# Kernel tuning notes

Measured on AMD Instinct MI355X. Metric: run time of the kernel, lower is better.

## Reference

```python
import jax, jax.numpy as jnp
import numpy as np

N = 100_000      # n_nodes
E = 1_000_000    # n_edges (avg degree 10)
DIN = 64
DOUT = 64


def setup_inputs() -> dict:
    key = jax.random.key(0)
    k1, k2, k3, k4 = jax.random.split(key, 4)
    x = jax.random.normal(k1, (N, DIN), dtype=jnp.float32)
    edge_index = jax.random.randint(k2, (2, E), 0, N, dtype=jnp.int32)
    # GCNConv linear weight (glorot-ish scale) and bias
    W = jax.random.normal(k3, (DIN, DOUT), dtype=jnp.float32) * (1.0 / np.sqrt(DIN))
    b = jax.random.normal(k4, (DOUT,), dtype=jnp.float32) * 0.01
    return {"x": x, "edge_index": edge_index, "W": W, "b": b}


def reference(x, edge_index, W, b):
    n = x.shape[0]
    # linear transform first (PyG GCNConv: x = self.lin(x))
    h = x @ W  # [N, DOUT]
    # add self-loops
    loop = jnp.arange(n, dtype=edge_index.dtype)
    row = jnp.concatenate([edge_index[0], loop])  # source j
    col = jnp.concatenate([edge_index[1], loop])  # target i
    # symmetric normalization: deg computed on target index (PyG gcn_norm)
    deg = jax.ops.segment_sum(jnp.ones(row.shape[0], dtype=h.dtype), col, num_segments=n)
    dinv = jnp.where(deg > 0, jax.lax.rsqrt(deg), 0.0)
    norm = dinv[row] * dinv[col]  # [E+N]
    # gather source features, scale, scatter-add to targets
    out = jax.ops.segment_sum(norm[:, None] * h[row], col, num_segments=n)
    out = out + b
    # dropout is identity in eval mode; act = relu
    return jax.nn.relu(out)
```

## Files before the change

### kernel.cpp

```cpp
#include <hip/hip_runtime.h>
#include <hip/hip_bf16.h>

#define F 64
#define BK 64
#define CAP 1024
#define ECAP 1024
#define KMAX 1600
#define PA_BLOCKS 512

typedef __attribute__((ext_vector_type(8))) short bf16x8;
typedef __attribute__((ext_vector_type(4))) float f32x4;

static __device__ inline short f2bf_bits(float f) {
    union { __hip_bfloat16 b; short s; } cv;
    cv.b = __float2bfloat16(f);
    return cv.s;
}

static __device__ inline float bf_lo(unsigned u) { return __uint_as_float(u << 16); }
static __device__ inline float bf_hi(unsigned u) { return __uint_as_float(u & 0xffff0000u); }

struct Acc8 {
    float a0, a1, a2, a3, a4, a5, a6, a7;
    __device__ inline void fma8(float wt, uint4 hv) {
        a0 += wt * bf_lo(hv.x);
        a1 += wt * bf_hi(hv.x);
        a2 += wt * bf_lo(hv.y);
        a3 += wt * bf_hi(hv.y);
        a4 += wt * bf_lo(hv.z);
        a5 += wt * bf_hi(hv.z);
        a6 += wt * bf_lo(hv.w);
        a7 += wt * bf_hi(hv.w);
    }
};

__global__ void __launch_bounds__(256)
k1_kernel(const float* __restrict__ x, const float* __restrict__ W,
          __hip_bfloat16* __restrict__ h,
          const int* __restrict__ row, const int* __restrict__ col,
          int* __restrict__ bcursor, unsigned* __restrict__ bin,
          int n, int e, int ngemm, int K, int chunk) {
    __shared__ int smem[2 * KMAX];
    int tid = threadIdx.x;

    if ((int)blockIdx.x < ngemm) {
        short* Wb = (short*)smem;
        for (int i = tid; i < F * F; i += 256) Wb[i] = f2bf_bits(W[i]);
        __syncthreads();
        int lane = tid & 63;
        int wv = tid >> 6;
        int quad = lane >> 4;
        int l16 = lane & 15;

        bf16x8 bfr[2][4];
#pragma unroll
        for (int ks = 0; ks < 2; ++ks)
#pragma unroll
            for (int nb = 0; nb < 4; ++nb) {
                bf16x8 f;
#pragma unroll
                for (int j = 0; j < 8; ++j)
                    f[j] = Wb[(ks * 32 + quad * 8 + j) * F + nb * 16 + l16];
                bfr[ks][nb] = f;
            }

        int blockbase = blockIdx.x * 128;
#pragma unroll
        for (int mt = 0; mt < 2; ++mt) {
            int trow = blockbase + (wv * 2 + mt) * 16;
            int ar = trow + l16;
            bf16x8 af0, af1;
            if (ar < n) {
                const float* xr = x + (size_t)ar * F + quad * 8;
                float4 v0 = ((const float4*)xr)[0];
                float4 v1 = ((const float4*)xr)[1];
                float4 v2 = ((const float4*)(xr + 32))[0];
                float4 v3 = ((const float4*)(xr + 32))[1];
                af0[0] = f2bf_bits(v0.x); af0[1] = f2bf_bits(v0.y);
                af0[2] = f2bf_bits(v0.z); af0[3] = f2bf_bits(v0.w);
                af0[4] = f2bf_bits(v1.x); af0[5] = f2bf_bits(v1.y);
                af0[6] = f2bf_bits(v1.z); af0[7] = f2bf_bits(v1.w);
                af1[0] = f2bf_bits(v2.x); af1[1] = f2bf_bits(v2.y);
                af1[2] = f2bf_bits(v2.z); af1[3] = f2bf_bits(v2.w);
                af1[4] = f2bf_bits(v3.x); af1[5] = f2bf_bits(v3.y);
                af1[6] = f2bf_bits(v3.z); af1[7] = f2bf_bits(v3.w);
            } else {
                af0 = (bf16x8)0; af1 = (bf16x8)0;
            }
            f32x4 acc[4];
#pragma unroll
            for (int nb = 0; nb < 4; ++nb) {
                acc[nb] = (f32x4)0.f;
                acc[nb] = __builtin_amdgcn_mfma_f32_16x16x32_bf16(af0, bfr[0][nb], acc[nb], 0, 0, 0);
                acc[nb] = __builtin_amdgcn_mfma_f32_16x16x32_bf16(af1, bfr[1][nb], acc[nb], 0, 0, 0);
            }
#pragma unroll
            for (int nb = 0; nb < 4; ++nb)
#pragma unroll
                for (int r = 0; r < 4; ++r) {
                    int grow = trow + quad * 4 + r;
                    if (grow < n)
                        h[(size_t)grow * F + nb * 16 + l16] = __float2bfloat16(acc[nb][r]);
                }
        }
    } else {
        int* lh = smem;
        int* lbase = smem + KMAX;
        int pb = blockIdx.x - ngemm;
        int s = pb * chunk;
        int lim = min(s + chunk, e);
        for (int i = tid; i < K; i += 256) lh[i] = 0;
        __syncthreads();
        for (int i = s + tid; i < lim; i += 256) atomicAdd(&lh[col[i] >> 6], 1);
        __syncthreads();
        for (int i = tid; i < K; i += 256) {
            int c = lh[i];
            lbase[i] = c ? atomicAdd(&bcursor[i], c) : 0;
            lh[i] = 0;
        }
        __syncthreads();
        for (int i = s + tid; i < lim; i += 256) {
            int d = col[i];
            int bkt = d >> 6;
            int off = lbase[bkt] + atomicAdd(&lh[bkt], 1);
            if (off < CAP)
                bin[(size_t)bkt * CAP + off] = ((unsigned)row[i] << 6) | ((unsigned)d & 63u);
        }
    }
}

__global__ void __launch_bounds__(256)
dinv_kernel(const unsigned* __restrict__ bin, const int* __restrict__ bcursor,
            float* __restrict__ dinv, int n) {
    __shared__ int lcnt[BK];
    int tid = threadIdx.x;
    int b = blockIdx.x;
    int s = b * CAP;
    int cnt = min(bcursor[b], ECAP);
    if (tid < BK) lcnt[tid] = 0;
    __syncthreads();
    for (int p = tid; p < cnt; p += 256) atomicAdd(&lcnt[bin[s + p] & 63u], 1);
    __syncthreads();
    if (tid < BK) {
        int node = (b << 6) + tid;
        if (node < n) dinv[node] = rsqrtf((float)(lcnt[tid] + 1));
    }
}

__global__ void __launch_bounds__(256)
gather_kernel(const unsigned* __restrict__ bin, const int* __restrict__ bcursor,
              const float* __restrict__ dinv, const __hip_bfloat16* __restrict__ h,
              const float* __restrict__ bias, float* __restrict__ out, int n) {
    __shared__ unsigned ebuf[ECAP];
    __shared__ uint2 sent[ECAP];
    __shared__ int lcnt[BK];
    __shared__ int sstart[BK];
    __shared__ int lcur[BK];
    __shared__ int sc[BK];
    __shared__ float sdinv[BK];
    int tid = threadIdx.x;
    int b = blockIdx.x;
    int base = b << 6;
    int s = b * CAP;
    int cnt = min(bcursor[b], ECAP);

    if (tid < BK) lcnt[tid] = 0;
    __syncthreads();
    for (int p = tid; p < cnt; p += 256) {
        unsigned u = bin[s + p];
        ebuf[p] = u;
        atomicAdd(&lcnt[u & 63u], 1);
    }
    __syncthreads();
    if (tid < BK) sc[tid] = lcnt[tid];
    __syncthreads();
    for (int off = 1; off < BK; off <<= 1) {
        int t = (tid < BK && tid >= off) ? sc[tid - off] : 0;
        __syncthreads();
        if (tid < BK) sc[tid] += t;
        __syncthreads();
    }
    if (tid < BK) {
        int c = lcnt[tid];
        int st = sc[tid] - c;
        sstart[tid] = st;
        lcur[tid] = st;
        sdinv[tid] = rsqrtf((float)(c + 1));
    }
    __syncthreads();
    for (int p = tid; p < cnt; p += 256) {
        unsigned u = ebuf[p];
        int src = (int)(u >> 6);
        float w = dinv[src];
        int pos = atomicAdd(&lcur[u & 63u], 1);
        sent[pos] = make_uint2((unsigned)src, __float_as_uint(w));
    }
    __syncthreads();

    int g = tid >> 3, cl = tid & 7;
    const uint4* h8 = (const uint4*)h;
#pragma unroll
    for (int r = 0; r < 2; ++r) {
        int ln = r * 32 + g;
        int node = base + ln;
        if (node >= n) continue;
        float di = sdinv[ln];
        Acc8 ac = {0.f, 0.f, 0.f, 0.f, 0.f, 0.f, 0.f, 0.f};
        {
            uint4 hv = h8[(size_t)node * 8 + cl];
            ac.fma8(di, hv);
        }
        int p = sstart[ln];
        int pend = p + lcnt[ln];
        for (; p + 4 <= pend; p += 4) {
            uint2 e0 = sent[p];
            uint2 e1 = sent[p + 1];
            uint2 e2 = sent[p + 2];
            uint2 e3 = sent[p + 3];
            uint4 v0 = h8[(size_t)e0.x * 8 + cl];
            uint4 v1 = h8[(size_t)e1.x * 8 + cl];
            uint4 v2 = h8[(size_t)e2.x * 8 + cl];
            uint4 v3 = h8[(size_t)e3.x * 8 + cl];
            ac.fma8(__uint_as_float(e0.y), v0);
            ac.fma8(__uint_as_float(e1.y), v1);
            ac.fma8(__uint_as_float(e2.y), v2);
            ac.fma8(__uint_as_float(e3.y), v3);
        }
        for (; p < pend; ++p) {
            uint2 ew = sent[p];
            uint4 hv = h8[(size_t)ew.x * 8 + cl];
            ac.fma8(__uint_as_float(ew.y), hv);
        }
        float4 b0 = ((const float4*)bias)[cl * 2];
        float4 b1 = ((const float4*)bias)[cl * 2 + 1];
        float4 r0, r1;
        r0.x = di * ac.a0 + b0.x; r0.y = di * ac.a1 + b0.y;
        r0.z = di * ac.a2 + b0.z; r0.w = di * ac.a3 + b0.w;
        r1.x = di * ac.a4 + b1.x; r1.y = di * ac.a5 + b1.y;
        r1.z = di * ac.a6 + b1.z; r1.w = di * ac.a7 + b1.w;
        r0.x = r0.x > 0.f ? r0.x : 0.f; r0.y = r0.y > 0.f ? r0.y : 0.f;
        r0.z = r0.z > 0.f ? r0.z : 0.f; r0.w = r0.w > 0.f ? r0.w : 0.f;
        r1.x = r1.x > 0.f ? r1.x : 0.f; r1.y = r1.y > 0.f ? r1.y : 0.f;
        r1.z = r1.z > 0.f ? r1.z : 0.f; r1.w = r1.w > 0.f ? r1.w : 0.f;
        ((float4*)out)[(size_t)node * 16 + cl * 2] = r0;
        ((float4*)out)[(size_t)node * 16 + cl * 2 + 1] = r1;
    }
}

extern "C" void kernel_launch(void* const* d_in, const int* in_sizes, int n_in,
                              void* d_out, int out_size, void* d_ws, size_t ws_size,
                              hipStream_t stream) {
    const float* x = (const float*)d_in[0];
    const int* ei  = (const int*)d_in[1];
    const float* W = (const float*)d_in[2];
    const float* b = (const float*)d_in[3];
    float* out = (float*)d_out;

    int n = in_sizes[0] / F;
    int e = in_sizes[1] / 2;
    const int* row = ei;
    const int* col = ei + e;
    int K = (n + BK - 1) / BK;

    __hip_bfloat16* h = (__hip_bfloat16*)d_ws;
    unsigned* bin = (unsigned*)((char*)d_ws + (size_t)n * F * 2);
    float* dinv   = (float*)(bin + (size_t)KMAX * CAP);
    int* bcursor  = (int*)(dinv + n);

    (void)hipMemsetAsync(bcursor, 0, KMAX * sizeof(int), stream);

    int ngemm = (n + 127) / 128;
    int chunk = (e + PA_BLOCKS - 1) / PA_BLOCKS;
    k1_kernel<<<ngemm + PA_BLOCKS, 256, 0, stream>>>(x, W, h, row, col, bcursor,
                                                     bin, n, e, ngemm, K, chunk);

    dinv_kernel<<<K, 256, 0, stream>>>(bin, bcursor, dinv, n);

    gather_kernel<<<K, 256, 0, stream>>>(bin, bcursor, dinv, h, b, out, n);
}
```

Before: 135.4 us.

## Privatize per-wave degree histograms, use shuffle scan, degree-sort nodes in gather

The degree histograms in dinv_kernel and gather_kernel are split into four per-wave copies to cut LDS atomic contention, then summed. The barrier-heavy shared-memory prefix scan is replaced by a wave-level __shfl_up scan. Each node is also ranked by degree and the gather loop walks nodes in that sorted order, so the 8-lane groups within a wave handle neighbor lists of similar length and diverge less. The cost is an extra O(64) rank loop per block and a little more shared memory.

```diff
diff --git a/kernel.cpp b/kernel.cpp
--- a/kernel.cpp
+++ b/kernel.cpp
@@ -132,18 +132,20 @@
 __global__ void __launch_bounds__(256)
 dinv_kernel(const unsigned* __restrict__ bin, const int* __restrict__ bcursor,
             float* __restrict__ dinv, int n) {
-    __shared__ int lcnt[BK];
+    __shared__ int lcnt4[4][BK];
     int tid = threadIdx.x;
     int b = blockIdx.x;
     int s = b * CAP;
     int cnt = min(bcursor[b], ECAP);
-    if (tid < BK) lcnt[tid] = 0;
-    __syncthreads();
-    for (int p = tid; p < cnt; p += 256) atomicAdd(&lcnt[bin[s + p] & 63u], 1);
+    ((int*)lcnt4)[tid] = 0;
+    __syncthreads();
+    int wvid = tid >> 6;
+    for (int p = tid; p < cnt; p += 256) atomicAdd(&lcnt4[wvid][bin[s + p] & 63u], 1);
     __syncthreads();
     if (tid < BK) {
+        int c = lcnt4[0][tid] + lcnt4[1][tid] + lcnt4[2][tid] + lcnt4[3][tid];
         int node = (b << 6) + tid;
-        if (node < n) dinv[node] = rsqrtf((float)(lcnt[tid] + 1));
+        if (node < n) dinv[node] = rsqrtf((float)(c + 1));
     }
 }
 
@@ -153,39 +155,46 @@
               const float* __restrict__ bias, float* __restrict__ out, int n) {
     __shared__ unsigned ebuf[ECAP];
     __shared__ uint2 sent[ECAP];
+    __shared__ int lcnt4[4][BK];
     __shared__ int lcnt[BK];
     __shared__ int sstart[BK];
     __shared__ int lcur[BK];
-    __shared__ int sc[BK];
     __shared__ float sdinv[BK];
+    __shared__ unsigned char order_[BK];
     int tid = threadIdx.x;
     int b = blockIdx.x;
     int base = b << 6;
     int s = b * CAP;
     int cnt = min(bcursor[b], ECAP);
-
-    if (tid < BK) lcnt[tid] = 0;
+    int wvid = tid >> 6;
+
+    ((int*)lcnt4)[tid] = 0;
     __syncthreads();
     for (int p = tid; p < cnt; p += 256) {
         unsigned u = bin[s + p];
         ebuf[p] = u;
-        atomicAdd(&lcnt[u & 63u], 1);
-    }
-    __syncthreads();
-    if (tid < BK) sc[tid] = lcnt[tid];
-    __syncthreads();
-    for (int off = 1; off < BK; off <<= 1) {
-        int t = (tid < BK && tid >= off) ? sc[tid - off] : 0;
-        __syncthreads();
-        if (tid < BK) sc[tid] += t;
-        __syncthreads();
-    }
+        atomicAdd(&lcnt4[wvid][u & 63u], 1);
+    }
+    __syncthreads();
     if (tid < BK) {
-        int c = lcnt[tid];
-        int st = sc[tid] - c;
+        int c = lcnt4[0][tid] + lcnt4[1][tid] + lcnt4[2][tid] + lcnt4[3][tid];
+        lcnt[tid] = c;
+        int scv = c;
+#pragma unroll
+        for (int off = 1; off < BK; off <<= 1) {
+            int t = __shfl_up(scv, off, 64);
+            if (tid >= off) scv += t;
+        }
+        int st = scv - c;
         sstart[tid] = st;
         lcur[tid] = st;
         sdinv[tid] = rsqrtf((float)(c + 1));
+        int rk = 0;
+        for (int j = 0; j < BK; ++j) {
+            int cj = lcnt[j];
+            rk += (cj < c) || (cj == c && j < tid);
+        }
+        order_[rk] = (unsigned char)tid;
     }
     __syncthreads();
     for (int p = tid; p < cnt; p += 256) {
@@ -201,7 +210,7 @@
     const uint4* h8 = (const uint4*)h;
 #pragma unroll
     for (int r = 0; r < 2; ++r) {
-        int ln = r * 32 + g;
+        int ln = order_[r * 32 + g];
         int node = base + ln;
         if (node >= n) continue;
         float di = sdinv[ln];
```

Result: slower. 141.8 us (+4.7%).

## Fold degree counting into first kernel with global atomics, drop dinv kernel

Applied to the files above, without the earlier changes.

Removes the separate dinv kernel launch by adding extra blocks to the fused GEMM/binning kernel that count in-degrees with global atomicAdd on col. The gather kernel then computes the source normalization as rsqrt(deg+1) on the fly instead of reading a precomputed dinv array. This saves one launch and one pass over the binned edges, but adds about a million global atomics that contend with the GEMM and binning blocks, plus a larger memset.

```diff
diff --git a/kernel.cpp b/kernel.cpp
--- a/kernel.cpp
+++ b/kernel.cpp
@@ -7,6 +7,7 @@
 #define ECAP 1024
 #define KMAX 1600
 #define PA_BLOCKS 512
+#define DEG_BLOCKS 256
 
 typedef __attribute__((ext_vector_type(8))) short bf16x8;
 typedef __attribute__((ext_vector_type(4))) float f32x4;
@@ -38,8 +39,9 @@
 k1_kernel(const float* __restrict__ x, const float* __restrict__ W,
           __hip_bfloat16* __restrict__ h,
           const int* __restrict__ row, const int* __restrict__ col,
-          int* __restrict__ bcursor, unsigned* __restrict__ bin,
-          int n, int e, int ngemm, int K, int chunk) {
+          int* __restrict__ bcursor, int* __restrict__ deg,
+          unsigned* __restrict__ bin,
+          int n, int e, int ngemm, int K, int chunk, int dchunk) {
     __shared__ int smem[2 * KMAX];
     int tid = threadIdx.x;
 
@@ -103,7 +105,7 @@
                         h[(size_t)grow * F + nb * 16 + l16] = __float2bfloat16(acc[nb][r]);
                 }
         }
-    } else {
+    } else if ((int)blockIdx.x < ngemm + PA_BLOCKS) {
         int* lh = smem;
         int* lbase = smem + KMAX;
         int pb = blockIdx.x - ngemm;
@@ -126,30 +128,18 @@
             if (off < CAP)
                 bin[(size_t)bkt * CAP + off] = ((unsigned)row[i] << 6) | ((unsigned)d & 63u);
         }
-    }
-}
-
-__global__ void __launch_bounds__(256)
-dinv_kernel(const unsigned* __restrict__ bin, const int* __restrict__ bcursor,
-            float* __restrict__ dinv, int n) {
-    __shared__ int lcnt[BK];
-    int tid = threadIdx.x;
-    int b = blockIdx.x;
-    int s = b * CAP;
-    int cnt = min(bcursor[b], ECAP);
-    if (tid < BK) lcnt[tid] = 0;
-    __syncthreads();
-    for (int p = tid; p < cnt; p += 256) atomicAdd(&lcnt[bin[s + p] & 63u], 1);
-    __syncthreads();
-    if (tid < BK) {
-        int node = (b << 6) + tid;
-        if (node < n) dinv[node] = rsqrtf((float)(lcnt[tid] + 1));
+    } else {
+        int db = blockIdx.x - ngemm - PA_BLOCKS;
+        int s = db * dchunk;
+        int lim = min(s + dchunk, e);
+        for (int i = s + tid; i < lim; i += 256)
+            atomicAdd(&deg[col[i]], 1);
     }
 }
 
 __global__ void __launch_bounds__(256)
 gather_kernel(const unsigned* __restrict__ bin, const int* __restrict__ bcursor,
-              const float* __restrict__ dinv, const __hip_bfloat16* __restrict__ h,
+              const int* __restrict__ deg, const __hip_bfloat16* __restrict__ h,
               const float* __restrict__ bias, float* __restrict__ out, int n) {
     __shared__ unsigned ebuf[ECAP];
     __shared__ uint2 sent[ECAP];
@@ -191,7 +181,7 @@
     for (int p = tid; p < cnt; p += 256) {
         unsigned u = ebuf[p];
         int src = (int)(u >> 6);
-        float w = dinv[src];
+        float w = rsqrtf((float)(deg[src] + 1));
         int pos = atomicAdd(&lcur[u & 63u], 1);
         sent[pos] = make_uint2((unsigned)src, __float_as_uint(w));
     }
@@ -264,17 +254,16 @@
 
     __hip_bfloat16* h = (__hip_bfloat16*)d_ws;
     unsigned* bin = (unsigned*)((char*)d_ws + (size_t)n * F * 2);
-    float* dinv   = (float*)(bin + (size_t)KMAX * CAP);
-    int* bcursor  = (int*)(dinv + n);
-
-    (void)hipMemsetAsync(bcursor, 0, KMAX * sizeof(int), stream);
+    int* deg      = (int*)(bin + (size_t)KMAX * CAP);
+    int* bcursor  = deg + n;
+
+    (void)hipMemsetAsync(deg, 0, (size_t)(n + KMAX) * sizeof(int), stream);
 
     int ngemm = (n + 127) / 128;
     int chunk = (e + PA_BLOCKS - 1) / PA_BLOCKS;
-    k1_kernel<<<ngemm + PA_BLOCKS, 256, 0, stream>>>(x, W, h, row, col, bcursor,
-                                                     bin, n, e, ngemm, K, chunk);
-
-    dinv_kernel<<<K, 256, 0, stream>>>(bin, bcursor, dinv, n);
-
-    gather_kernel<<<K, 256, 0, stream>>>(bin, bcursor, dinv, h, b, out, n);
-}
+    int dchunk = (e + DEG_BLOCKS - 1) / DEG_BLOCKS;
+    k1_kernel<<<ngemm + PA_BLOCKS + DEG_BLOCKS, 256, 0, stream>>>(
+        x, W, h, row, col, bcursor, deg, bin, n, e, ngemm, K, chunk, dchunk);
+
+    gather_kernel<<<K, 256, 0, stream>>>(bin, bcursor, deg, h, b, out, n);
+}
```

Result: slower. 170.3 us (+25.8%).

## Fuse dinv and gather kernels into one cooperative kernel with grid sync

Applied to the files above, without the earlier changes.

Replaces the separate dinv and gather launches with a single cooperative kernel. Each block reads its bucket's edges once into LDS, computes the degree and dinv, publishes dinv, waits on a grid-wide barrier, then gathers neighbour features. The aim is to cut one launch and the second global read of the bin array. In exchange it adds a grid sync and an occupancy query on the host, and the occupancy check (max blocks per CU times 256 against K) looks like an approximation that may not guarantee co-residency.

```diff
diff --git a/kernel.cpp b/kernel.cpp
--- a/kernel.cpp
+++ b/kernel.cpp
@@ -1,5 +1,8 @@
 #include <hip/hip_runtime.h>
 #include <hip/hip_bf16.h>
+#include <hip/hip_cooperative_groups.h>
+
+namespace cg = cooperative_groups;
 
 #define F 64
 #define BK 64
@@ -129,6 +132,105 @@
     }
 }
 
+__global__ void __launch_bounds__(256, 8)
+fused_kernel(const unsigned* __restrict__ bin, const int* __restrict__ bcursor,
+             float* __restrict__ dinv, const __hip_bfloat16* __restrict__ h,
+             const float* __restrict__ bias, float* __restrict__ out, int n) {
+    __shared__ unsigned ebuf[ECAP];
+    __shared__ uint2 sent[ECAP];
+    __shared__ int lcnt[BK];
+    __shared__ int sstart[BK];
+    __shared__ int lcur[BK];
+    __shared__ int sc[BK];
+    __shared__ float sdinv[BK];
+    int tid = threadIdx.x;
+    int b = blockIdx.x;
+    int base = b << 6;
+    int s = b * CAP;
+    int cnt = min(bcursor[b], ECAP);
+
+    if (tid < BK) lcnt[tid] = 0;
+    __syncthreads();
+    for (int p = tid; p < cnt; p += 256) {
+        unsigned u = bin[s + p];
+        ebuf[p] = u;
+        atomicAdd(&lcnt[u & 63u], 1);
+    }
+    __syncthreads();
+    if (tid < BK) sc[tid] = lcnt[tid];
+    __syncthreads();
+    for (int off = 1; off < BK; off <<= 1) {
+        int t = (tid < BK && tid >= off) ? sc[tid - off] : 0;
+        __syncthreads();
+        if (tid < BK) sc[tid] += t;
+        __syncthreads();
+    }
+    if (tid < BK) {
+        int c = lcnt[tid];
+        int st = sc[tid] - c;
+        sstart[tid] = st;
+        lcur[tid] = st;
+        float dv = rsqrtf((float)(c + 1));
+        sdinv[tid] = dv;
+        int node = base + tid;
+        if (node < n) dinv[node] = dv;
+    }
+
+    cg::this_grid().sync();
+
+    for (int p = tid; p < cnt; p += 256) {
+        unsigned u = ebuf[p];
+        int src = (int)(u >> 6);
+        float w = dinv[src];
+        int pos = atomicAdd(&lcur[u & 63u], 1);
+        sent[pos] = make_uint2((unsigned)src, __float_as_uint(w));
+    }
+    __syncthreads();
+
+    int g = tid >> 3, cl = tid & 7;
+    const uint4* h8 = (const uint4*)h;
+#pragma unroll
+    for (int r = 0; r < 2; ++r) {
+        int ln = r * 32 + g;
+        int node = base + ln;
+        if (node >= n) continue;
+        float di = sdinv[ln];
+        Acc8 ac = {0.f, 0.f, 0.f, 0.f, 0.f, 0.f, 0.f, 0.f};
+        {
+            uint4 hv = h8[(size_t)node * 8 + cl];
+            ac.fma8(di, hv);
+        }
+        int p = sstart[ln];
+        int pend = p + lcnt[ln];
+        for (; p + 2 <= pend; p += 2) {
+            uint2 e0 = sent[p];
+            uint2 e1 = sent[p + 1];
+            uint4 v0 = h8[(size_t)e0.x * 8 + cl];
+            uint4 v1 = h8[(size_t)e1.x * 8 + cl];
+            ac.fma8(__uint_as_float(e0.y), v0);
+            ac.fma8(__uint_as_float(e1.y), v1);
+        }
+        if (p < pend) {
+            uint2 ew = sent[p];
+            uint4 hv = h8[(size_t)ew.x * 8 + cl];
+            ac.fma8(__uint_as_float(ew.y), hv);
+        }
+        float4 b0 = ((const float4*)bias)[cl * 2];
+        float4 b1 = ((const float4*)bias)[cl * 2 + 1];
+        float4 r0, r1;
+        r0.x = di * ac.a0 + b0.x; r0.y = di * ac.a1 + b0.y;
+        r0.z = di * ac.a2 + b0.z; r0.w = di * ac.a3 + b0.w;
+        r1.x = di * ac.a4 + b1.x; r1.y = di * ac.a5 + b1.y;
+        r1.z = di * ac.a6 + b1.z; r1.w = di * ac.a7 + b1.w;
+        r0.x = r0.x > 0.f ? r0.x : 0.f; r0.y = r0.y > 0.f ? r0.y : 0.f;
+        r0.z = r0.z > 0.f ? r0.z : 0.f; r0.w = r0.w > 0.f ? r0.w : 0.f;
+        r1.x = r1.x > 0.f ? r1.x : 0.f; r1.y = r1.y > 0.f ? r1.y : 0.f;
+        r1.z = r1.z > 0.f ? r1.z : 0.f; r1.w = r1.w > 0.f ? r1.w : 0.f;
+        ((float4*)out)[(size_t)node * 16 + cl * 2] = r0;
+        ((float4*)out)[(size_t)node * 16 + cl * 2 + 1] = r1;
+    }
+}
+
 __global__ void __launch_bounds__(256)
 dinv_kernel(const unsigned* __restrict__ bin, const int* __restrict__ bcursor,
             float* __restrict__ dinv, int n) {
@@ -274,7 +376,17 @@
     k1_kernel<<<ngemm + PA_BLOCKS, 256, 0, stream>>>(x, W, h, row, col, bcursor,
                                                      bin, n, e, ngemm, K, chunk);
 
+    int maxBlocksPerCU = 0;
+    hipError_t occErr = hipOccupancyMaxActiveBlocksPerMultiprocessor(
+        &maxBlocksPerCU, fused_kernel, 256, 0);
+    bool coop = (occErr == hipSuccess) && ((long)maxBlocksPerCU * 256 >= (long)K);
+    if (coop) {
+        void* args[] = {(void*)&bin, (void*)&bcursor, (void*)&dinv, (void*)&h,
+                        (void*)&b, (void*)&out, (void*)&n};
+        hipError_t lerr = hipLaunchCooperativeKernel((void*)fused_kernel, dim3(K),
+                                                     dim3(256), args, 0, stream);
+        if (lerr == hipSuccess) return;
+    }
     dinv_kernel<<<K, 256, 0, stream>>>(bin, bcursor, dinv, n);
-
     gather_kernel<<<K, 256, 0, stream>>>(bin, bcursor, dinv, h, b, out, n);
 }
```

After: 136.9 us. No clear change (+1.1%).
